# Optimization experiments

Measured on AMD Instinct MI355X. Metric: run time of the kernel, lower is better.

Reference implementation:

```python
import jax, jax.numpy as jnp
import numpy as np

H, M, D, O, N = 16, 1024, 512, 512, 16384


def setup_inputs() -> dict:
    key = jax.random.key(0)
    ks = jax.random.split(key, 8)
    inp = {
        "k": jax.random.normal(ks[0], (N, O), dtype=jnp.float32),
        "mems": jax.random.normal(ks[1], (H, M, D), dtype=jnp.float32),
        "Wk": jax.random.normal(ks[2], (H, O, D), dtype=jnp.float32) * (1.0 / np.sqrt(D)),
        "bk": jax.random.normal(ks[3], (H, O), dtype=jnp.float32) * 0.02,
        "Wv": jax.random.normal(ks[4], (H, O, D), dtype=jnp.float32) * (1.0 / np.sqrt(D)),
        "bv": jax.random.normal(ks[5], (H, O), dtype=jnp.float32) * 0.02,
        "Wf": jax.random.normal(ks[6], (O, H * O), dtype=jnp.float32) * (1.0 / np.sqrt(H * O)),
        "bf": jax.random.normal(ks[7], (O,), dtype=jnp.float32) * 0.02,
    }
    return inp


def reference(k, mems, Wk, bk, Wv, bv, Wf, bf):
    # Batched over heads. Per head h:
    #   key_h = softmax(mem_h @ Wk_h^T + bk_h)  -> [M, O]
    #   val_h = mem_h @ Wv_h^T + bv_h           -> [M, O]
    #   att_h = softmax(k @ key_h^T)            -> [N, M]
    #   out_h = att_h @ val_h                   -> [N, O]
    key_logits = jnp.einsum("hmd,hod->hmo", mems, Wk) + bk[:, None, :]
    mem_key = jax.nn.softmax(key_logits, axis=-1)            # [H, M, O]
    mem_val = jnp.einsum("hmd,hod->hmo", mems, Wv) + bv[:, None, :]  # [H, M, O]
    att = jnp.einsum("no,hmo->hnm", k, mem_key)              # [H, N, M]
    att_w = jax.nn.softmax(att, axis=-1)
    out_h = jnp.einsum("hnm,hmo->hno", att_w, mem_val)       # [H, N, O]
    # torch.cat(outputs, dim=-1): head h occupies columns [h*O:(h+1)*O]
    x = jnp.transpose(out_h, (1, 0, 2)).reshape(N, H * O)    # [N, H*O]
    return x @ Wf.T + bf                                     # [N, O]
```

## Files before the change

### kernel.cpp

```cpp
#include <hip/hip_runtime.h>
#include <math.h>

typedef unsigned short u16;
typedef __attribute__((ext_vector_type(8))) short short8;
typedef __attribute__((ext_vector_type(4))) float floatx4;

#define Hh 16
#define Mm 1024
#define Dd 512
#define Oo 512
#define Nn 16384

__device__ __forceinline__ float b2f(u16 u) { return __uint_as_float(((unsigned)u) << 16); }
__device__ __forceinline__ u16 f2b(float f) {
    unsigned v = __float_as_uint(f);
    v += 0x7fffu + ((v >> 16) & 1u);
    return (u16)(v >> 16);
}
__device__ __forceinline__ short8 cvt8(const float* p) {
    float4 a = *(const float4*)p, b = *(const float4*)(p + 4);
    u16 o[8];
    o[0] = f2b(a.x); o[1] = f2b(a.y); o[2] = f2b(a.z); o[3] = f2b(a.w);
    o[4] = f2b(b.x); o[5] = f2b(b.y); o[6] = f2b(b.z); o[7] = f2b(b.w);
    return *(short8*)o;
}

__global__ __launch_bounds__(256) void gemm_bt(
    const void* __restrict__ A, const void* __restrict__ B, const float* __restrict__ bias,
    void* __restrict__ C, int K, int lda, int ldb, int ldc,
    long sA, long sB, long sBias, long sC, int aF32, int bF32, int outBf)
{
    __shared__ u16 At[64][72];
    __shared__ u16 Bt[64][72];
    const int tid = threadIdx.x, lane = tid & 63, wid = tid >> 6;
    const int m0 = blockIdx.y * 64, n0 = blockIdx.x * 64;
    const int h = blockIdx.z;
    const int wm = wid >> 1, wn = wid & 1;
    const int rl = lane & 15, rq = (lane >> 4) * 4, gl8 = (lane >> 4) * 8;

    floatx4 zero4 = {0.f, 0.f, 0.f, 0.f};
    floatx4 acc[2][2];
    acc[0][0] = zero4; acc[0][1] = zero4; acc[1][0] = zero4; acc[1][1] = zero4;

    for (int k0 = 0; k0 < K; k0 += 64) {
#pragma unroll
        for (int i = 0; i < 2; i++) {
            int c = tid + i * 256;
            int r = c >> 3, cc = (c & 7) * 8;
            long aoff = (long)h * sA + (long)(m0 + r) * lda + k0 + cc;
            long boff = (long)h * sB + (long)(n0 + r) * ldb + k0 + cc;
            *(short8*)&At[r][cc] = aF32 ? cvt8((const float*)A + aoff)
                                        : *(const short8*)((const u16*)A + aoff);
            *(short8*)&Bt[r][cc] = bF32 ? cvt8((const float*)B + boff)
                                        : *(const short8*)((const u16*)B + boff);
        }
        __syncthreads();
#pragma unroll
        for (int ks = 0; ks < 2; ks++) {
            short8 a0 = *(const short8*)&At[wm * 32 + rl][ks * 32 + gl8];
            short8 a1 = *(const short8*)&At[wm * 32 + 16 + rl][ks * 32 + gl8];
            short8 b0 = *(const short8*)&Bt[wn * 32 + rl][ks * 32 + gl8];
            short8 b1 = *(const short8*)&Bt[wn * 32 + 16 + rl][ks * 32 + gl8];
            acc[0][0] = __builtin_amdgcn_mfma_f32_16x16x32_bf16(a0, b0, acc[0][0], 0, 0, 0);
            acc[0][1] = __builtin_amdgcn_mfma_f32_16x16x32_bf16(a0, b1, acc[0][1], 0, 0, 0);
            acc[1][0] = __builtin_amdgcn_mfma_f32_16x16x32_bf16(a1, b0, acc[1][0], 0, 0, 0);
            acc[1][1] = __builtin_amdgcn_mfma_f32_16x16x32_bf16(a1, b1, acc[1][1], 0, 0, 0);
        }
        __syncthreads();
    }

#pragma unroll
    for (int i = 0; i < 2; i++)
#pragma unroll
        for (int j = 0; j < 2; j++) {
            int col = n0 + wn * 32 + j * 16 + rl;
            float bb = bias ? bias[(long)h * sBias + col] : 0.f;
#pragma unroll
            for (int r = 0; r < 4; r++) {
                int row = m0 + wm * 32 + i * 16 + rq + r;
                long idx = (long)h * sC + (long)row * ldc + col;
                float v = acc[i][j][r] + bb;
                if (outBf) ((u16*)C)[idx] = f2b(v);
                else       ((float*)C)[idx] = v;
            }
        }
}

__global__ __launch_bounds__(256) void softmax_rows(const float* __restrict__ L, u16* __restrict__ Kout)
{
    const int tid = threadIdx.x, lane = tid & 63, wid = tid >> 6;
    const long row = (long)blockIdx.x * 4 + wid;
    const float* p = L + row * 512 + lane * 8;
    float v[8];
    *(float4*)&v[0] = *(const float4*)p;
    *(float4*)&v[4] = *(const float4*)(p + 4);
    float mx = v[0];
#pragma unroll
    for (int i = 1; i < 8; i++) mx = fmaxf(mx, v[i]);
    for (int d = 1; d < 64; d <<= 1) mx = fmaxf(mx, __shfl_xor(mx, d));
    float s = 0.f;
#pragma unroll
    for (int i = 0; i < 8; i++) { v[i] = __expf(v[i] - mx); s += v[i]; }
    for (int d = 1; d < 64; d <<= 1) s += __shfl_xor(s, d);
    float inv = 1.f / s;
    u16 o[8];
#pragma unroll
    for (int i = 0; i < 8; i++) o[i] = f2b(v[i] * inv);
    *(short8*)(Kout + row * 512 + lane * 8) = *(short8*)o;
}

#define LDQ 520
#define LDP 516
#define FLASH_LDS (64 * LDQ * 2 + 64 * LDP * 2 + 2 * 64 * 4 + 16)

__global__ __launch_bounds__(1024) void flash(
    const float* __restrict__ kq, const u16* __restrict__ key,
    const u16* __restrict__ vpt, const float* __restrict__ bfv, float* __restrict__ out)
{
    extern __shared__ u16 sm[];
    u16* kq_s = sm;
    u16* Ph = sm + 64 * LDQ;
    float* lbuf = (float*)(sm + 64 * (LDQ + LDP));

    const int tid = threadIdx.x, lane = tid & 63, wid = tid >> 6;
    const int n0 = blockIdx.x * 64;
    const int rl = lane & 15, rq = (lane >> 4) * 4, gl8 = (lane >> 4) * 8;

#pragma unroll
    for (int i = 0; i < 4; i++) {
        int c = tid + i * 1024;
        int r = c >> 6, cc = (c & 63) * 8;
        *(short8*)&kq_s[r * LDQ + cc] = cvt8(&kq[(long)(n0 + r) * 512 + cc]);
    }
    if (tid < 128) lbuf[tid] = 0.f;
    __syncthreads();

    floatx4 zero4 = {0.f, 0.f, 0.f, 0.f};
    floatx4 oacc[4][2], utmp[4][2];
#pragma unroll
    for (int i = 0; i < 4; i++)
#pragma unroll
        for (int j = 0; j < 2; j++) { oacc[i][j] = zero4; utmp[i][j] = zero4; }

    for (int h = 0; h < Hh; h++) {
        const u16* keyh = key + (long)h * Mm * Oo;
        const u16* vph = vpt + (long)h * Oo * Mm;
        float* lcur = lbuf + (h & 1) * 64;
        float* lnxt = lbuf + ((h + 1) & 1) * 64;

        for (int hf = 0; hf < 2; hf++) {
            float psum[4][4];
#pragma unroll
            for (int qt = 0; qt < 4; qt++)
#pragma unroll
                for (int r = 0; r < 4; r++) psum[qt][r] = 0.f;

#pragma unroll
            for (int t = 0; t < 2; t++) {
                int mb = hf * 512 + wid * 32 + t * 16;
                const u16* bp = keyh + (long)(mb + rl) * 512 + gl8;
                floatx4 s[4];
#pragma unroll
                for (int qt = 0; qt < 4; qt++) s[qt] = zero4;
#pragma unroll
                for (int ks = 0; ks < 16; ks++) {
                    short8 b = *(const short8*)(bp + ks * 32);
#pragma unroll
                    for (int qt = 0; qt < 4; qt++) {
                        short8 a = *(const short8*)&kq_s[(qt * 16 + rl) * LDQ + ks * 32 + gl8];
                        s[qt] = __builtin_amdgcn_mfma_f32_16x16x32_bf16(a, b, s[qt], 0, 0, 0);
                    }
                }
                int colP = wid * 32 + t * 16 + rl;
#pragma unroll
                for (int qt = 0; qt < 4; qt++)
#pragma unroll
                    for (int r = 0; r < 4; r++) {
                        float e = __expf(s[qt][r]);
                        psum[qt][r] += e;
                        Ph[(qt * 16 + rq + r) * LDP + colP] = f2b(e);
                    }
            }
            for (int d = 1; d < 16; d <<= 1)
#pragma unroll
                for (int qt = 0; qt < 4; qt++)
#pragma unroll
                    for (int r = 0; r < 4; r++) psum[qt][r] += __shfl_xor(psum[qt][r], d);
            if (rl == 0)
#pragma unroll
                for (int qt = 0; qt < 4; qt++)
#pragma unroll
                    for (int r = 0; r < 4; r++)
                        atomicAdd(&lcur[qt * 16 + rq + r], psum[qt][r]);
            if (hf == 0 && tid < 64) lnxt[tid] = 0.f;
            __syncthreads();

            const u16* vbp[2];
#pragma unroll
            for (int ot = 0; ot < 2; ot++)
                vbp[ot] = vph + (long)(wid * 32 + ot * 16 + rl) * Mm + hf * 512 + gl8;
#pragma unroll 4
            for (int mk = 0; mk < 16; mk++) {
                short8 a[4], b[2];
#pragma unroll
                for (int qt = 0; qt < 4; qt++)
                    a[qt] = *(const short8*)&Ph[(qt * 16 + rl) * LDP + mk * 32 + gl8];
#pragma unroll
                for (int ot = 0; ot < 2; ot++)
                    b[ot] = *(const short8*)(vbp[ot] + mk * 32);
#pragma unroll
                for (int qt = 0; qt < 4; qt++)
#pragma unroll
                    for (int ot = 0; ot < 2; ot++)
                        utmp[qt][ot] = __builtin_amdgcn_mfma_f32_16x16x32_bf16(a[qt], b[ot], utmp[qt][ot], 0, 0, 0);
            }

            if (hf == 1) {
#pragma unroll
                for (int qt = 0; qt < 4; qt++)
#pragma unroll
                    for (int r = 0; r < 4; r++) {
                        float inv = 1.f / lcur[qt * 16 + rq + r];
#pragma unroll
                        for (int ot = 0; ot < 2; ot++) {
                            oacc[qt][ot][r] += inv * utmp[qt][ot][r];
                            utmp[qt][ot][r] = 0.f;
                        }
                    }
            }
            __syncthreads();
        }
    }

#pragma unroll
    for (int qt = 0; qt < 4; qt++)
#pragma unroll
        for (int ot = 0; ot < 2; ot++) {
            int col = wid * 32 + ot * 16 + rl;
            float add = bfv[col];
#pragma unroll
            for (int r = 0; r < 4; r++) {
                int row = n0 + qt * 16 + rq + r;
                out[(long)row * 512 + col] = oacc[qt][ot][r] + add;
            }
        }
}

extern "C" void kernel_launch(void* const* d_in, const int* in_sizes, int n_in,
                              void* d_out, int out_size, void* d_ws, size_t ws_size,
                              hipStream_t stream)
{
    const float* k    = (const float*)d_in[0];
    const void*  mems = d_in[1];
    const void*  Wk   = d_in[2];
    const float* bk   = (const float*)d_in[3];
    const void*  Wv   = d_in[4];
    const float* bv   = (const float*)d_in[5];
    const void*  Wf   = d_in[6];
    const float* bfv  = (const float*)d_in[7];
    float* out = (float*)d_out;

    char* ws = (char*)d_ws;
    float* logits = (float*)ws;
    u16* keyb = (u16*)(ws + (size_t)Hh * Mm * Oo * 4);
    u16* valb = keyb + (size_t)Hh * Mm * Oo;
    u16* vptb = valb + (size_t)Hh * Mm * Oo;

    gemm_bt<<<dim3(8, 16, 16), 256, 0, stream>>>(
        mems, Wk, bk, logits, 512, 512, 512, 512,
        (long)Mm * Dd, (long)Oo * Dd, 512L, (long)Mm * Oo, 1, 1, 0);

    softmax_rows<<<dim3(Hh * Mm / 4), 256, 0, stream>>>(logits, keyb);

    gemm_bt<<<dim3(8, 16, 16), 256, 0, stream>>>(
        mems, Wv, bv, valb, 512, 512, 512, 512,
        (long)Mm * Dd, (long)Oo * Dd, 512L, (long)Mm * Oo, 1, 1, 1);

    gemm_bt<<<dim3(16, 8, 16), 256, 0, stream>>>(
        Wf, valb, nullptr, vptb, 512, Hh * Oo, 512, 1024,
        512L, (long)Mm * Oo, 0L, (long)Oo * Mm, 1, 0, 1);

    flash<<<dim3(Nn / 64), 1024, FLASH_LDS, stream>>>(k, keyb, vptb, bfv, out);
}
```

Baseline: 1.758 ms.

## Split fused flash kernel into materialized S-GEMM and PV-GEMM passes over head groups

```diff
diff --git a/kernel.cpp b/kernel.cpp
--- a/kernel.cpp
+++ b/kernel.cpp
@@ -2,6 +2,7 @@
 #include <math.h>
 
 typedef unsigned short u16;
+typedef unsigned int u32;
 typedef __attribute__((ext_vector_type(8))) short short8;
 typedef __attribute__((ext_vector_type(4))) float floatx4;
 
@@ -10,8 +11,8 @@
 #define Dd 512
 #define Oo 512
 #define Nn 16384
-
-__device__ __forceinline__ float b2f(u16 u) { return __uint_as_float(((unsigned)u) << 16); }
+#define GRP 2
+
 __device__ __forceinline__ u16 f2b(float f) {
     unsigned v = __float_as_uint(f);
     v += 0x7fffu + ((v >> 16) & 1u);
@@ -23,6 +24,12 @@
     o[0] = f2b(a.x); o[1] = f2b(a.y); o[2] = f2b(a.z); o[3] = f2b(a.w);
     o[4] = f2b(b.x); o[5] = f2b(b.y); o[6] = f2b(b.z); o[7] = f2b(b.w);
     return *(short8*)o;
+}
+
+__device__ __forceinline__ void gl_lds16(const u16* g, u16* lds) {
+    __builtin_amdgcn_global_load_lds(
+        (const __attribute__((address_space(1))) u32*)g,
+        (__attribute__((address_space(3))) u32*)lds, 16, 0, 0);
 }
 
 __global__ __launch_bounds__(256) void gemm_bt(
@@ -109,139 +116,183 @@
     *(short8*)(Kout + row * 512 + lane * 8) = *(short8*)o;
 }
 
-#define LDQ 520
-#define LDP 516
-#define FLASH_LDS (64 * LDQ * 2 + 64 * LDP * 2 + 2 * 64 * 4 + 16)
-
-__global__ __launch_bounds__(1024) void flash(
-    const float* __restrict__ kq, const u16* __restrict__ key,
-    const u16* __restrict__ vpt, const float* __restrict__ bfv, float* __restrict__ out)
-{
-    extern __shared__ u16 sm[];
-    u16* kq_s = sm;
-    u16* Ph = sm + 64 * LDQ;
-    float* lbuf = (float*)(sm + 64 * (LDQ + LDP));
-
+__global__ __launch_bounds__(256) void cvt_zero(
+    const float* __restrict__ in, u16* __restrict__ ob, float* __restrict__ lz)
+{
+    long i = ((long)blockIdx.x * 256 + threadIdx.x) * 8;
+    *(short8*)(ob + i) = cvt8(in + i);
+    if (blockIdx.x < 256) {
+        long j = ((long)blockIdx.x * 256 + threadIdx.x) * 4;
+        float4 z = {0.f, 0.f, 0.f, 0.f};
+        *(float4*)(lz + j) = z;
+    }
+}
+
+__global__ __launch_bounds__(256) void s_gemm(
+    const u16* __restrict__ A,
+    const u16* __restrict__ B,
+    u16* __restrict__ P,
+    float* __restrict__ l,
+    int h0)
+{
+    __shared__ u16 Asl[128 * 64];
+    __shared__ u16 Bsl[128 * 64];
     const int tid = threadIdx.x, lane = tid & 63, wid = tid >> 6;
-    const int n0 = blockIdx.x * 64;
-    const int rl = lane & 15, rq = (lane >> 4) * 4, gl8 = (lane >> 4) * 8;
-
-#pragma unroll
-    for (int i = 0; i < 4; i++) {
-        int c = tid + i * 1024;
-        int r = c >> 6, cc = (c & 63) * 8;
-        *(short8*)&kq_s[r * LDQ + cc] = cvt8(&kq[(long)(n0 + r) * 512 + cc]);
-    }
-    if (tid < 128) lbuf[tid] = 0.f;
-    __syncthreads();
+    const int n0 = blockIdx.x * 128, m0 = blockIdx.y * 128;
+    const int hg = blockIdx.z, h = h0 + hg;
+    const int wr = wid >> 1, wc = wid & 1;
+    const int rl = lane & 15, rq = (lane >> 4) * 4, g8 = (lane >> 4) * 8;
+    const int lrow = lane >> 3, lcol8 = (lane & 7) * 8;
+    const u16* Bh = B + (long)h * Mm * Dd;
 
     floatx4 zero4 = {0.f, 0.f, 0.f, 0.f};
-    floatx4 oacc[4][2], utmp[4][2];
-#pragma unroll
-    for (int i = 0; i < 4; i++)
-#pragma unroll
-        for (int j = 0; j < 2; j++) { oacc[i][j] = zero4; utmp[i][j] = zero4; }
-
-    for (int h = 0; h < Hh; h++) {
-        const u16* keyh = key + (long)h * Mm * Oo;
-        const u16* vph = vpt + (long)h * Oo * Mm;
-        float* lcur = lbuf + (h & 1) * 64;
-        float* lnxt = lbuf + ((h + 1) & 1) * 64;
-
-        for (int hf = 0; hf < 2; hf++) {
-            float psum[4][4];
-#pragma unroll
-            for (int qt = 0; qt < 4; qt++)
-#pragma unroll
-                for (int r = 0; r < 4; r++) psum[qt][r] = 0.f;
-
-#pragma unroll
-            for (int t = 0; t < 2; t++) {
-                int mb = hf * 512 + wid * 32 + t * 16;
-                const u16* bp = keyh + (long)(mb + rl) * 512 + gl8;
-                floatx4 s[4];
-#pragma unroll
-                for (int qt = 0; qt < 4; qt++) s[qt] = zero4;
-#pragma unroll
-                for (int ks = 0; ks < 16; ks++) {
-                    short8 b = *(const short8*)(bp + ks * 32);
-#pragma unroll
-                    for (int qt = 0; qt < 4; qt++) {
-                        short8 a = *(const short8*)&kq_s[(qt * 16 + rl) * LDQ + ks * 32 + gl8];
-                        s[qt] = __builtin_amdgcn_mfma_f32_16x16x32_bf16(a, b, s[qt], 0, 0, 0);
-                    }
-                }
-                int colP = wid * 32 + t * 16 + rl;
-#pragma unroll
-                for (int qt = 0; qt < 4; qt++)
-#pragma unroll
-                    for (int r = 0; r < 4; r++) {
-                        float e = __expf(s[qt][r]);
-                        psum[qt][r] += e;
-                        Ph[(qt * 16 + rq + r) * LDP + colP] = f2b(e);
-                    }
-            }
-            for (int d = 1; d < 16; d <<= 1)
-#pragma unroll
-                for (int qt = 0; qt < 4; qt++)
-#pragma unroll
-                    for (int r = 0; r < 4; r++) psum[qt][r] += __shfl_xor(psum[qt][r], d);
-            if (rl == 0)
-#pragma unroll
-                for (int qt = 0; qt < 4; qt++)
-#pragma unroll
-                    for (int r = 0; r < 4; r++)
-                        atomicAdd(&lcur[qt * 16 + rq + r], psum[qt][r]);
-            if (hf == 0 && tid < 64) lnxt[tid] = 0.f;
+    floatx4 acc[4][4];
+#pragma unroll
+    for (int i = 0; i < 4; i++)
+#pragma unroll
+        for (int j = 0; j < 4; j++) acc[i][j] = zero4;
+
+    for (int k0 = 0; k0 < 512; k0 += 64) {
+#pragma unroll
+        for (int s = 0; s < 8; s++) {
+            int t = wid * 8 + s;
+            int r0 = (t & 15) * 8;
+            if (t < 16) gl_lds16(A  + (long)(m0 + r0 + lrow) * 512 + k0 + lcol8, &Asl[r0 * 64]);
+            else        gl_lds16(Bh + (long)(n0 + r0 + lrow) * 512 + k0 + lcol8, &Bsl[r0 * 64]);
+        }
+        asm volatile("s_waitcnt vmcnt(0)" ::: "memory");
+        __syncthreads();
+#pragma unroll
+        for (int ks = 0; ks < 2; ks++) {
+            short8 af[4], bfr[4];
+#pragma unroll
+            for (int i = 0; i < 4; i++)
+                af[i] = *(const short8*)&Asl[(wr * 64 + i * 16 + rl) * 64 + ks * 32 + g8];
+#pragma unroll
+            for (int j = 0; j < 4; j++)
+                bfr[j] = *(const short8*)&Bsl[(wc * 64 + j * 16 + rl) * 64 + ks * 32 + g8];
+#pragma unroll
+            for (int i = 0; i < 4; i++)
+#pragma unroll
+                for (int j = 0; j < 4; j++)
+                    acc[i][j] = __builtin_amdgcn_mfma_f32_16x16x32_bf16(af[i], bfr[j], acc[i][j], 0, 0, 0);
+        }
+        __syncthreads();
+    }
+
+    u16* Pt = P + (long)hg * Nn * Mm;
+    float rsum[4][4];
+#pragma unroll
+    for (int i = 0; i < 4; i++)
+#pragma unroll
+        for (int r = 0; r < 4; r++) rsum[i][r] = 0.f;
+#pragma unroll
+    for (int i = 0; i < 4; i++)
+#pragma unroll
+        for (int j = 0; j < 4; j++) {
+            int col = n0 + wc * 64 + j * 16 + rl;
+#pragma unroll
+            for (int r = 0; r < 4; r++) {
+                int row = m0 + wr * 64 + i * 16 + rq + r;
+                float e = __expf(acc[i][j][r]);
+                Pt[(long)row * Mm + col] = f2b(e);
+                rsum[i][r] += e;
+            }
+        }
+    for (int d = 1; d < 16; d <<= 1)
+#pragma unroll
+        for (int i = 0; i < 4; i++)
+#pragma unroll
+            for (int r = 0; r < 4; r++) rsum[i][r] += __shfl_xor(rsum[i][r], d);
+    if (rl == 0)
+#pragma unroll
+        for (int i = 0; i < 4; i++)
+#pragma unroll
+            for (int r = 0; r < 4; r++)
+                atomicAdd(&l[(long)h * Nn + m0 + wr * 64 + i * 16 + rq + r], rsum[i][r]);
+}
+
+__global__ __launch_bounds__(256) void pv_gemm(
+    const u16* __restrict__ P,
+    const u16* __restrict__ V,
+    const float* __restrict__ l,
+    const float* __restrict__ bfv,
+    float* __restrict__ out,
+    int h0, int first)
+{
+    __shared__ u16 Asl[128 * 64];
+    __shared__ u16 Bsl[128 * 64];
+    const int tid = threadIdx.x, lane = tid & 63, wid = tid >> 6;
+    const int n0 = blockIdx.x * 128, m0 = blockIdx.y * 128;
+    const int wr = wid >> 1, wc = wid & 1;
+    const int rl = lane & 15, rq = (lane >> 4) * 4, g8 = (lane >> 4) * 8;
+    const int lrow = lane >> 3, lcol8 = (lane & 7) * 8;
+
+    floatx4 zero4 = {0.f, 0.f, 0.f, 0.f};
+    floatx4 acc[4][4];
+#pragma unroll
+    for (int i = 0; i < 4; i++)
+#pragma unroll
+        for (int j = 0; j < 4; j++) acc[i][j] = zero4;
+
+    for (int hg = 0; hg < GRP; hg++) {
+        const int h = h0 + hg;
+        const u16* Ah = P + (long)hg * Nn * Mm;
+        const u16* Bh = V + (long)h * Oo * Mm;
+        floatx4 a2[4][4];
+#pragma unroll
+        for (int i = 0; i < 4; i++)
+#pragma unroll
+            for (int j = 0; j < 4; j++) a2[i][j] = zero4;
+
+        for (int k0 = 0; k0 < Mm; k0 += 64) {
+#pragma unroll
+            for (int s = 0; s < 8; s++) {
+                int t = wid * 8 + s;
+                int r0 = (t & 15) * 8;
+                if (t < 16) gl_lds16(Ah + (long)(m0 + r0 + lrow) * Mm + k0 + lcol8, &Asl[r0 * 64]);
+                else        gl_lds16(Bh + (long)(n0 + r0 + lrow) * Mm + k0 + lcol8, &Bsl[r0 * 64]);
+            }
+            asm volatile("s_waitcnt vmcnt(0)" ::: "memory");
             __syncthreads();
-
-            const u16* vbp[2];
-#pragma unroll
-            for (int ot = 0; ot < 2; ot++)
-                vbp[ot] = vph + (long)(wid * 32 + ot * 16 + rl) * Mm + hf * 512 + gl8;
-#pragma unroll 4
-            for (int mk = 0; mk < 16; mk++) {
-                short8 a[4], b[2];
-#pragma unroll
-                for (int qt = 0; qt < 4; qt++)
-                    a[qt] = *(const short8*)&Ph[(qt * 16 + rl) * LDP + mk * 32 + gl8];
-#pragma unroll
-                for (int ot = 0; ot < 2; ot++)
-                    b[ot] = *(const short8*)(vbp[ot] + mk * 32);
-#pragma unroll
-                for (int qt = 0; qt < 4; qt++)
-#pragma unroll
-                    for (int ot = 0; ot < 2; ot++)
-                        utmp[qt][ot] = __builtin_amdgcn_mfma_f32_16x16x32_bf16(a[qt], b[ot], utmp[qt][ot], 0, 0, 0);
-            }
-
-            if (hf == 1) {
-#pragma unroll
-                for (int qt = 0; qt < 4; qt++)
-#pragma unroll
-                    for (int r = 0; r < 4; r++) {
-                        float inv = 1.f / lcur[qt * 16 + rq + r];
-#pragma unroll
-                        for (int ot = 0; ot < 2; ot++) {
-                            oacc[qt][ot][r] += inv * utmp[qt][ot][r];
-                            utmp[qt][ot][r] = 0.f;
-                        }
-                    }
+#pragma unroll
+            for (int ks = 0; ks < 2; ks++) {
+                short8 af[4], bfr[4];
+#pragma unroll
+                for (int i = 0; i < 4; i++)
+                    af[i] = *(const short8*)&Asl[(wr * 64 + i * 16 + rl) * 64 + ks * 32 + g8];
+#pragma unroll
+                for (int j = 0; j < 4; j++)
+                    bfr[j] = *(const short8*)&Bsl[(wc * 64 + j * 16 + rl) * 64 + ks * 32 + g8];
+#pragma unroll
+                for (int i = 0; i < 4; i++)
+#pragma unroll
+                    for (int j = 0; j < 4; j++)
+                        a2[i][j] = __builtin_amdgcn_mfma_f32_16x16x32_bf16(af[i], bfr[j], a2[i][j], 0, 0, 0);
             }
             __syncthreads();
         }
-    }
-
-#pragma unroll
-    for (int qt = 0; qt < 4; qt++)
-#pragma unroll
-        for (int ot = 0; ot < 2; ot++) {
-            int col = wid * 32 + ot * 16 + rl;
-            float add = bfv[col];
+#pragma unroll
+        for (int i = 0; i < 4; i++)
 #pragma unroll
             for (int r = 0; r < 4; r++) {
-                int row = n0 + qt * 16 + rq + r;
-                out[(long)row * 512 + col] = oacc[qt][ot][r] + add;
+                float inv = 1.f / l[(long)h * Nn + m0 + wr * 64 + i * 16 + rq + r];
+#pragma unroll
+                for (int j = 0; j < 4; j++) acc[i][j][r] += inv * a2[i][j][r];
+            }
+    }
+
+#pragma unroll
+    for (int i = 0; i < 4; i++)
+#pragma unroll
+        for (int j = 0; j < 4; j++) {
+            int col = n0 + wc * 64 + j * 16 + rl;
+#pragma unroll
+            for (int r = 0; r < 4; r++) {
+                int row = m0 + wr * 64 + i * 16 + rq + r;
+                long idx = (long)row * Oo + col;
+                float base = first ? bfv[col] : out[idx];
+                out[idx] = base + acc[i][j][r];
             }
         }
 }
@@ -261,10 +312,14 @@
     float* out = (float*)d_out;
 
     char* ws = (char*)d_ws;
-    float* logits = (float*)ws;
-    u16* keyb = (u16*)(ws + (size_t)Hh * Mm * Oo * 4);
-    u16* valb = keyb + (size_t)Hh * Mm * Oo;
-    u16* vptb = valb + (size_t)Hh * Mm * Oo;
+    u16*   keyb   = (u16*)ws;
+    u16*   vptb   = (u16*)(ws + (size_t)Hh * Mm * Oo * 2);
+    u16*   kqb    = (u16*)(ws + (size_t)Hh * Mm * Oo * 4);
+    float* lbuf   = (float*)(ws + (size_t)Hh * Mm * Oo * 4 + (size_t)Nn * Dd * 2);
+    char*  pbase  = ws + (size_t)Hh * Mm * Oo * 4 + (size_t)Nn * Dd * 2 + (size_t)Hh * Nn * 4;
+    u16*   Pbuf   = (u16*)pbase;
+    float* logits = (float*)pbase;
+    u16*   valb   = (u16*)(pbase + (size_t)Hh * Mm * Oo * 4);
 
     gemm_bt<<<dim3(8, 16, 16), 256, 0, stream>>>(
         mems, Wk, bk, logits, 512, 512, 512, 512,
@@ -280,5 +335,12 @@
         Wf, valb, nullptr, vptb, 512, Hh * Oo, 512, 1024,
         512L, (long)Mm * Oo, 0L, (long)Oo * Mm, 1, 0, 1);
 
-    flash<<<dim3(Nn / 64), 1024, FLASH_LDS, stream>>>(k, keyb, vptb, bfv, out);
-}
+    cvt_zero<<<dim3(Nn * Dd / (256 * 8)), 256, 0, stream>>>(k, kqb, lbuf);
+
+    for (int g = 0; g < Hh / GRP; g++) {
+        s_gemm<<<dim3(Mm / 128, Nn / 128, GRP), 256, 0, stream>>>(
+            kqb, keyb, Pbuf, lbuf, g * GRP);
+        pv_gemm<<<dim3(Oo / 128, Nn / 128, 1), 256, 0, stream>>>(
+            Pbuf, vptb, lbuf, bfv, out, g * GRP, g == 0);
+    }
+}
```

Result: faster. 1.693 ms (-3.7%).
